# Kernel optimization log

Hardware: AMD Instinct MI355X
Metric: run time of the kernel (lower is better)

## Reference

```python
import jax, jax.numpy as jnp
import numpy as np

B, S, D, H = 2, 2048, 1024, 16
DK = D // H  # 64
EPS = 1e-10
ROPE_BASE = 500000.0


def _rms_norm(x, w):
    # RMSNorm over last dim: w * x / sqrt(mean(x^2) + eps)
    return w * x * jax.lax.rsqrt(jnp.mean(x * x, axis=-1, keepdims=True) + EPS)


def _rope_tables(seq_len, dk):
    inv_freq = 1.0 / (ROPE_BASE ** (jnp.arange(0, dk, 2, dtype=jnp.float32) / dk))
    t = jnp.arange(seq_len, dtype=jnp.float32)
    freqs = jnp.outer(t, inv_freq)            # (S, dk/2)
    emb = jnp.concatenate([freqs, freqs], -1)  # (S, dk)
    return jnp.cos(emb), jnp.sin(emb)


def _rotate_half(x):
    x1, x2 = jnp.split(x, 2, axis=-1)
    return jnp.concatenate([-x2, x1], axis=-1)


def setup_inputs() -> dict:
    key = jax.random.key(0)
    ks = jax.random.split(key, 8)
    scale = 1.0 / np.sqrt(D)
    return {
        "q": jax.random.normal(ks[0], (B, S, D), jnp.float32),
        "k": jax.random.normal(ks[1], (B, S, D), jnp.float32),
        "v": jax.random.normal(ks[2], (B, S, D), jnp.float32),
        "Wq": jax.random.normal(ks[3], (D, D), jnp.float32) * scale,
        "Wk": jax.random.normal(ks[4], (D, D), jnp.float32) * scale,
        "Wv": jax.random.normal(ks[5], (D, D), jnp.float32) * scale,
        "Wo": jax.random.normal(ks[6], (D, D), jnp.float32) * scale,
        "q_norm_w": jnp.ones((DK,), jnp.float32) + 0.02 * jax.random.normal(ks[7], (DK,), jnp.float32),
        "k_norm_w": jnp.ones((DK,), jnp.float32),
    }


def reference(q, k, v, Wq, Wk, Wv, Wo, q_norm_w, k_norm_w):
    Bq, Sq, _ = q.shape
    # Projections (torch Linear: x @ W.T), split into heads -> (B, H, S, DK)
    def proj(x, W):
        return (x @ W.T).reshape(Bq, Sq, H, DK).transpose(0, 2, 1, 3)
    query, key_, value = proj(q, Wq), proj(k, Wk), proj(v, Wv)
    # Per-head QK RMSNorm
    query = _rms_norm(query, q_norm_w)
    key_ = _rms_norm(key_, k_norm_w)
    # RoPE
    cos, sin = _rope_tables(Sq, DK)  # (S, DK) each; broadcast over (B, H)
    query = query * cos + _rotate_half(query) * sin
    key_ = key_ * cos + _rotate_half(key_) * sin
    # Causal attention
    scale = 1.0 / np.sqrt(DK)
    scores = jnp.einsum("bhqd,bhkd->bhqk", query, key_) * scale
    causal = jnp.tril(jnp.ones((Sq, Sq), bool))
    scores = jnp.where(causal, scores, -jnp.inf)
    probs = jax.nn.softmax(scores, axis=-1)
    attn = jnp.einsum("bhqk,bhkd->bhqd", probs, value)
    # Merge heads and output projection
    attn = attn.transpose(0, 2, 1, 3).reshape(Bq, Sq, D)
    return attn @ Wo.T
```

## Files before the change

kernel.cpp:

```cpp
#include <hip/hip_runtime.h>
#include <hip/hip_bf16.h>
#include <math.h>

#define B_  2
#define S_  2048
#define D_  1024
#define H_  16
#define DK_ 64

typedef __attribute__((ext_vector_type(8))) short bf16x8;
typedef __attribute__((ext_vector_type(4))) float f32x4;
typedef __attribute__((ext_vector_type(4))) unsigned int u32x4;

#define MFMA_BF16(a, b, c) __builtin_amdgcn_mfma_f32_16x16x32_bf16((a), (b), (c), 0, 0, 0)

#define QSCALE 0.18033688011112042f
#define ROPE_L2 0.591611512f

__device__ __forceinline__ unsigned short f2bf(float f) {
  unsigned int u = __float_as_uint(f);
  u += 0x7FFFu + ((u >> 16) & 1u);
  return (unsigned short)(u >> 16);
}

__device__ __forceinline__ void gl_lds16(const void* g, void* l) {
  __builtin_amdgcn_global_load_lds(
      (const __attribute__((address_space(1))) void*)g,
      (__attribute__((address_space(3))) void*)l, 16, 0, 0);
}

__device__ __forceinline__ int lsw(int row, int col) {
  return row * 64 + ((((col) >> 3) ^ (row & 7)) << 3) + (col & 7);
}

__device__ __forceinline__ int vperm_inv(int c) {
  return (c & 32) | ((c & 8) << 1) | ((c & 4) << 1) | ((c & 16) >> 2);
}

__global__ __launch_bounds__(256)
void cvt_bf16(const float* __restrict__ q, const float* __restrict__ k,
              const float* __restrict__ v, const float* __restrict__ wq,
              const float* __restrict__ wk, const float* __restrict__ wv,
              const float* __restrict__ wo,
              unsigned short* __restrict__ qb, unsigned short* __restrict__ kb,
              unsigned short* __restrict__ vb, unsigned short* __restrict__ wqb,
              unsigned short* __restrict__ wkb, unsigned short* __restrict__ wvb,
              unsigned short* __restrict__ wob) {
  const float* src; unsigned short* dst; int n;
  switch (blockIdx.y) {
    case 0: src = q;  dst = qb;  n = B_ * S_ * D_; break;
    case 1: src = k;  dst = kb;  n = B_ * S_ * D_; break;
    case 2: src = v;  dst = vb;  n = B_ * S_ * D_; break;
    case 3: src = wq; dst = wqb; n = D_ * D_; break;
    case 4: src = wk; dst = wkb; n = D_ * D_; break;
    case 5: src = wv; dst = wvb; n = D_ * D_; break;
    default: src = wo; dst = wob; n = D_ * D_; break;
  }
  const int i = (blockIdx.x * 256 + threadIdx.x) * 4;
  if (i >= n) return;
  float4 val = *(const float4*)&src[i];
  ushort4 r4;
  r4.x = f2bf(val.x); r4.y = f2bf(val.y); r4.z = f2bf(val.z); r4.w = f2bf(val.w);
  *(ushort4*)&dst[i] = r4;
}

__global__ __launch_bounds__(256)
void gemm_qkv(const unsigned short* __restrict__ qa, const unsigned short* __restrict__ ka,
              const unsigned short* __restrict__ va,
              const unsigned short* __restrict__ wq, const unsigned short* __restrict__ wk,
              const unsigned short* __restrict__ wv,
              unsigned short* __restrict__ Qo, unsigned short* __restrict__ Ko,
              unsigned short* __restrict__ Vto,
              const float* __restrict__ qnw, const float* __restrict__ knw) {
  __shared__ unsigned short As[2][128 * 32];
  __shared__ unsigned short Bs[2][128 * 32];

  const int lin = blockIdx.x + (blockIdx.y << 3) + (blockIdx.z << 8);
  const int v_  = (lin & 7) * 96 + (lin >> 3);
  const int bx  = v_ & 7;
  const int panel = v_ >> 3;
  const int by  = panel & 31;
  const int z   = panel >> 5;

  const unsigned short* A = (z == 0) ? qa : (z == 1) ? ka : va;
  const unsigned short* W = (z == 0) ? wq : (z == 1) ? wk : wv;

  const int t = threadIdx.x, lane = t & 63, wave = t >> 6;
  const int l16 = lane & 15, quad = lane >> 4;
  const int wm = wave >> 1, wn = wave & 1;
  const int m0 = by * 128, j0 = bx * 128;

  f32x4 acc[4][4];
#pragma unroll
  for (int i = 0; i < 4; ++i)
#pragma unroll
    for (int j = 0; j < 4; ++j) acc[i][j] = (f32x4)(0.0f);

  auto stage = [&](int kb, int buf) {
#pragma unroll
    for (int i = 0; i < 2; ++i) {
      const int c  = (wave * 2 + i) * 64 + lane;
      const int r  = c >> 2;
      const int co = (c & 3) * 8;
      gl_lds16(&A[(size_t)(m0 + r) * D_ + kb + co], &As[buf][(wave * 2 + i) * 512]);
      gl_lds16(&W[(size_t)(j0 + r) * D_ + kb + co], &Bs[buf][(wave * 2 + i) * 512]);
    }
  };

  stage(0, 0);
  for (int kb = 0; kb < D_; kb += 32) {
    const int buf = (kb >> 5) & 1;
    __syncthreads();
    if (kb + 32 < D_) stage(kb + 32, buf ^ 1);

    bf16x8 af[4], bfr[4];
#pragma unroll
    for (int mi = 0; mi < 4; ++mi)
      af[mi] = *(const bf16x8*)&As[buf][(wm * 64 + mi * 16 + l16) * 32 + quad * 8];
#pragma unroll
    for (int ni = 0; ni < 4; ++ni)
      bfr[ni] = *(const bf16x8*)&Bs[buf][(wn * 64 + ni * 16 + l16) * 32 + quad * 8];
#pragma unroll
    for (int mi = 0; mi < 4; ++mi)
#pragma unroll
      for (int ni = 0; ni < 4; ++ni)
        acc[mi][ni] = MFMA_BF16(af[mi], bfr[ni], acc[mi][ni]);
  }

  const int h = bx * 2 + wn;
  if (z == 2) {
#pragma unroll
    for (int mi = 0; mi < 4; ++mi) {
      const int rowb = m0 + wm * 64 + mi * 16 + quad * 4;
      const int b = rowb >> 11, s0 = rowb & (S_ - 1);
      const int sp = (s0 & ~63) | vperm_inv(s0 & 63);
#pragma unroll
      for (int ni = 0; ni < 4; ++ni) {
        const int dk = ni * 16 + l16;
        const unsigned int u0 =
            (unsigned int)f2bf(acc[mi][ni][0]) | ((unsigned int)f2bf(acc[mi][ni][1]) << 16);
        const unsigned int u1 =
            (unsigned int)f2bf(acc[mi][ni][2]) | ((unsigned int)f2bf(acc[mi][ni][3]) << 16);
        *(uint2*)&Vto[((size_t)((b * H_ + h) * DK_ + dk)) * S_ + sp] = make_uint2(u0, u1);
      }
    }
  } else {
    unsigned short* out = (z == 0) ? Qo : Ko;
    const float* nw = (z == 0) ? qnw : knw;
    const float sc  = (z == 0) ? QSCALE : 1.0f;
    float wv_[4];
#pragma unroll
    for (int ni = 0; ni < 4; ++ni) wv_[ni] = nw[ni * 16 + l16];
    const float invA = exp2f(-(float)l16 * ROPE_L2);
    const float invB = exp2f(-(float)(16 + l16) * ROPE_L2);
#pragma unroll
    for (int mi = 0; mi < 4; ++mi) {
#pragma unroll
      for (int r = 0; r < 4; ++r) {
        const int rowg = m0 + wm * 64 + mi * 16 + quad * 4 + r;
        const int b = rowg >> 11, s = rowg & (S_ - 1);
        float ss = 0.f;
#pragma unroll
        for (int ni = 0; ni < 4; ++ni) ss += acc[mi][ni][r] * acc[mi][ni][r];
#pragma unroll
        for (int m = 1; m < 16; m <<= 1) ss += __shfl_xor(ss, m);
        const float rms = rsqrtf(ss * (1.0f / DK_) + 1e-10f);
        float xn[4];
#pragma unroll
        for (int ni = 0; ni < 4; ++ni) xn[ni] = wv_[ni] * acc[mi][ni][r] * rms;
        const float fA = (float)s * invA, fB = (float)s * invB;
        const float cA = __cosf(fA) * sc, sA = __sinf(fA) * sc;
        const float cB = __cosf(fB) * sc, sB = __sinf(fB) * sc;
        float o0 = xn[0] * cA - xn[2] * sA;
        float o1 = xn[1] * cB - xn[3] * sB;
        float o2 = xn[2] * cA + xn[0] * sA;
        float o3 = xn[3] * cB + xn[1] * sB;
        const size_t base = ((size_t)(b * H_ + h) * S_ + s) * DK_;
        out[base +  0 + l16] = f2bf(o0);
        out[base + 16 + l16] = f2bf(o1);
        out[base + 32 + l16] = f2bf(o2);
        out[base + 48 + l16] = f2bf(o3);
      }
    }
  }
}

__global__ __launch_bounds__(256)
void flash3(const unsigned short* __restrict__ Q, const unsigned short* __restrict__ K,
            const unsigned short* __restrict__ Vt, unsigned short* __restrict__ Oa) {
  __shared__ unsigned short Ks[2][64 * 64];
  __shared__ unsigned short Vs[3][64 * 64];
  const int bx = blockIdx.x;
  const int idx = bx >> 5;
  const int qt = (idx < 16) ? idx : (47 - idx);
  const int bh = bx & 31;
  const int t = threadIdx.x, lane = t & 63, wave = t >> 6;
  const int l16 = lane & 15, quad = lane >> 4;
  const size_t hb = (size_t)bh * S_ * DK_;
  const unsigned short* Qh  = Q + hb;
  const unsigned short* Kh  = K + hb;
  const unsigned short* Vth = Vt + hb;

  bf16x8 qf[2];
#pragma unroll
  for (int ks = 0; ks < 2; ++ks)
    qf[ks] = *(const bf16x8*)
      &Qh[(size_t)(qt * 64 + wave * 16 + l16) * DK_ + ks * 32 + quad * 8];

  bf16x8 ones;
#pragma unroll
  for (int j = 0; j < 8; ++j) ones[j] = (short)0x3F80;

  f32x4 o[4], lacc;
  lacc = (f32x4)(0.0f);
#pragma unroll
  for (int ni = 0; ni < 4; ++ni) o[ni] = (f32x4)(0.0f);

  auto stage = [&](int kt, int kb_, int vb_) {
#pragma unroll
    for (int i = 0; i < 2; ++i) {
      const int rbase = wave * 16 + i * 8;
      const int r = rbase + (lane >> 3);
      const int c = ((lane & 7) ^ (r & 7)) * 8;
      gl_lds16(&Kh[(size_t)(kt * 64 + r) * DK_ + c], &Ks[kb_][rbase * 64]);
      gl_lds16(&Vth[(size_t)r * S_ + kt * 64 + c], &Vs[vb_][rbase * 64]);
    }
  };

  f32x4 sv[4];

  auto qkt = [&](int kt) {
    const int buf = kt & 1;
#pragma unroll
    for (int kvi = 0; kvi < 4; ++kvi) sv[kvi] = (f32x4)(0.0f);
#pragma unroll
    for (int ks = 0; ks < 2; ++ks) {
      bf16x8 ak[4];
#pragma unroll
      for (int kvi = 0; kvi < 4; ++kvi)
        ak[kvi] = *(const bf16x8*)&Ks[buf][lsw(kvi * 16 + l16, ks * 32 + quad * 8)];
      __builtin_amdgcn_s_setprio(1);
#pragma unroll
      for (int kvi = 0; kvi < 4; ++kvi)
        sv[kvi] = MFMA_BF16(ak[kvi], qf[ks], sv[kvi]);
      __builtin_amdgcn_s_setprio(0);
    }
  };

  auto smx = [&](int kt, unsigned int (&pw)[4][2]) {
    if (kt == qt) {
      const int qg = qt * 64 + wave * 16 + l16;
#pragma unroll
      for (int kvi = 0; kvi < 4; ++kvi) {
        float e[4];
#pragma unroll
        for (int r = 0; r < 4; ++r) {
          float x = sv[kvi][r];
          if ((kt * 64 + kvi * 16 + quad * 4 + r) > qg) x = -INFINITY;
          e[r] = exp2f(x);
        }
        pw[kvi][0] = (__float_as_uint(e[1]) & 0xFFFF0000u) | (__float_as_uint(e[0]) >> 16);
        pw[kvi][1] = (__float_as_uint(e[3]) & 0xFFFF0000u) | (__float_as_uint(e[2]) >> 16);
      }
    } else {
#pragma unroll
      for (int kvi = 0; kvi < 4; ++kvi) {
        float e[4];
#pragma unroll
        for (int r = 0; r < 4; ++r) e[r] = exp2f(sv[kvi][r]);
        pw[kvi][0] = (__float_as_uint(e[1]) & 0xFFFF0000u) | (__float_as_uint(e[0]) >> 16);
        pw[kvi][1] = (__float_as_uint(e[3]) & 0xFFFF0000u) | (__float_as_uint(e[2]) >> 16);
      }
    }
  };

  auto pv = [&](const unsigned int (&pw)[4][2], int vb_) {
    bf16x8 ap[2];
#pragma unroll
    for (int ks = 0; ks < 2; ++ks) {
      u32x4 aw;
      aw.x = pw[2 * ks][0];
      aw.y = pw[2 * ks][1];
      aw.z = pw[2 * ks + 1][0];
      aw.w = pw[2 * ks + 1][1];
      ap[ks] = __builtin_bit_cast(bf16x8, aw);
    }
#pragma unroll
    for (int ks = 0; ks < 2; ++ks) {
      bf16x8 bv[4];
#pragma unroll
      for (int ni = 0; ni < 4; ++ni)
        bv[ni] = *(const bf16x8*)&Vs[vb_][lsw(ni * 16 + l16, ks * 32 + quad * 8)];
      __builtin_amdgcn_s_setprio(1);
#pragma unroll
      for (int ni = 0; ni < 4; ++ni)
        o[ni] = MFMA_BF16(ap[ks], bv[ni], o[ni]);
      lacc = MFMA_BF16(ap[ks], ones, lacc);
      __builtin_amdgcn_s_setprio(0);
    }
  };

  const int nkt = qt + 1;
  unsigned int pwA[4][2], pwB[4][2];

  stage(0, 0, 0);
  __syncthreads();
  if (nkt > 1) stage(1, 1, 1);
  qkt(0);
  smx(0, pwA);

  int kt = 1;
  for (; kt + 1 < nkt; kt += 2) {
    __syncthreads();
    stage(kt + 1, (kt + 1) & 1, (kt + 1) % 3);
    qkt(kt);
    pv(pwA, (kt - 1) % 3);
    smx(kt, pwB);
    __syncthreads();
    if (kt + 2 < nkt) stage(kt + 2, (kt + 2) & 1, (kt + 2) % 3);
    qkt(kt + 1);
    pv(pwB, kt % 3);
    smx(kt + 1, pwA);
  }
  if (kt < nkt) {
    __syncthreads();
    qkt(kt);
    pv(pwA, (kt - 1) % 3);
    smx(kt, pwB);
    pv(pwB, kt % 3);
  } else {
    pv(pwA, (nkt - 1) % 3);
  }

  const int b = bh >> 4, h = bh & 15;
#pragma unroll
  for (int r = 0; r < 4; ++r) {
    const int srow = qt * 64 + wave * 16 + quad * 4 + r;
    const float linv = 1.0f / lacc[r];
#pragma unroll
    for (int ni = 0; ni < 4; ++ni)
      Oa[((size_t)(b * S_ + srow) * H_ + h) * DK_ + ni * 16 + l16] =
          f2bf(o[ni][r] * linv);
  }
}

__global__ __launch_bounds__(256)
void gemm_out(const unsigned short* __restrict__ A, const unsigned short* __restrict__ W,
              float* __restrict__ out) {
  __shared__ unsigned short As[2][128 * 32];
  __shared__ unsigned short Bs[2][128 * 32];
  const int lin = blockIdx.x + (blockIdx.y << 3);
  const int v_  = (lin & 7) * 32 + (lin >> 3);
  const int bx  = v_ & 7;
  const int by  = v_ >> 3;

  const int t = threadIdx.x, lane = t & 63, wave = t >> 6;
  const int l16 = lane & 15, quad = lane >> 4;
  const int wm = wave >> 1, wn = wave & 1;
  const int m0 = by * 128, j0 = bx * 128;

  f32x4 acc[4][4];
#pragma unroll
  for (int i = 0; i < 4; ++i)
#pragma unroll
    for (int j = 0; j < 4; ++j) acc[i][j] = (f32x4)(0.0f);

  auto stage = [&](int kb, int buf) {
#pragma unroll
    for (int i = 0; i < 2; ++i) {
      const int c  = (wave * 2 + i) * 64 + lane;
      const int r  = c >> 2;
      const int co = (c & 3) * 8;
      gl_lds16(&A[(size_t)(m0 + r) * D_ + kb + co], &As[buf][(wave * 2 + i) * 512]);
      gl_lds16(&W[(size_t)(j0 + r) * D_ + kb + co], &Bs[buf][(wave * 2 + i) * 512]);
    }
  };

  stage(0, 0);
  for (int kb = 0; kb < D_; kb += 32) {
    const int buf = (kb >> 5) & 1;
    __syncthreads();
    if (kb + 32 < D_) stage(kb + 32, buf ^ 1);

    bf16x8 af[4], bfr[4];
#pragma unroll
    for (int mi = 0; mi < 4; ++mi)
      af[mi] = *(const bf16x8*)&As[buf][(wm * 64 + mi * 16 + l16) * 32 + quad * 8];
#pragma unroll
    for (int ni = 0; ni < 4; ++ni)
      bfr[ni] = *(const bf16x8*)&Bs[buf][(wn * 64 + ni * 16 + l16) * 32 + quad * 8];
#pragma unroll
    for (int mi = 0; mi < 4; ++mi)
#pragma unroll
      for (int ni = 0; ni < 4; ++ni)
        acc[mi][ni] = MFMA_BF16(af[mi], bfr[ni], acc[mi][ni]);
  }

#pragma unroll
  for (int mi = 0; mi < 4; ++mi) {
    const int rowb = m0 + wm * 64 + mi * 16 + quad * 4;
#pragma unroll
    for (int ni = 0; ni < 4; ++ni) {
      const int col = j0 + wn * 64 + ni * 16 + l16;
#pragma unroll
      for (int r = 0; r < 4; ++r)
        out[(size_t)(rowb + r) * D_ + col] = acc[mi][ni][r];
    }
  }
}

extern "C" void kernel_launch(void* const* d_in, const int* in_sizes, int n_in,
                              void* d_out, int out_size, void* d_ws, size_t ws_size,
                              hipStream_t stream) {
  (void)in_sizes; (void)n_in; (void)out_size; (void)ws_size;
  const float* q  = (const float*)d_in[0];
  const float* k  = (const float*)d_in[1];
  const float* v  = (const float*)d_in[2];
  const float* Wq = (const float*)d_in[3];
  const float* Wk = (const float*)d_in[4];
  const float* Wv = (const float*)d_in[5];
  const float* Wo = (const float*)d_in[6];
  const float* qw = (const float*)d_in[7];
  const float* kw = (const float*)d_in[8];

  char* ws = (char*)d_ws;
  const size_t MB = 1u << 20;
  unsigned short* qb  = (unsigned short*)(ws + 0 * MB);
  unsigned short* kb  = (unsigned short*)(ws + 8 * MB);
  unsigned short* vb  = (unsigned short*)(ws + 16 * MB);
  unsigned short* wqb = (unsigned short*)(ws + 24 * MB);
  unsigned short* wkb = (unsigned short*)(ws + 26 * MB);
  unsigned short* wvb = (unsigned short*)(ws + 28 * MB);
  unsigned short* wob = (unsigned short*)(ws + 30 * MB);
  unsigned short* Qb  = (unsigned short*)(ws + 32 * MB);
  unsigned short* Kb  = (unsigned short*)(ws + 40 * MB);
  unsigned short* Vtb = (unsigned short*)(ws + 48 * MB);
  unsigned short* Ab  = (unsigned short*)(ws + 56 * MB);

  cvt_bf16<<<dim3(4096, 7), 256, 0, stream>>>(q, k, v, Wq, Wk, Wv, Wo,
                                              qb, kb, vb, wqb, wkb, wvb, wob);

  gemm_qkv<<<dim3(D_ / 128, (B_ * S_) / 128, 3), 256, 0, stream>>>(
      qb, kb, vb, wqb, wkb, wvb, Qb, Kb, Vtb, qw, kw);

  flash3<<<1024, 256, 0, stream>>>(Qb, Kb, Vtb, Ab);

  gemm_out<<<dim3(D_ / 128, (B_ * S_) / 128), 256, 0, stream>>>(Ab, wob, (float*)d_out);
}
```

Measured before the change: 203.4 us.

## Fuse fp32-to-bf16 activation conversion into QKV GEMM tile loads

The separate conversion pass over the q/k/v activations is removed. The QKV GEMM now streams fp32 activation tiles directly into a swizzled LDS buffer and converts them to bf16 by truncation when building MFMA fragments. This drops a full read and write of three large activation tensors and the extra kernel work. In exchange the GEMM loads twice as many bytes for A per tile, uses more LDS, and rounds by truncation instead of round-to-nearest.

```diff
diff --git a/kernel.cpp b/kernel.cpp
--- a/kernel.cpp
+++ b/kernel.cpp
@@ -23,6 +23,10 @@
   return (unsigned short)(u >> 16);
 }
 
+__device__ __forceinline__ unsigned int packtr(float e0, float e1) {
+  return (__float_as_uint(e1) & 0xFFFF0000u) | (__float_as_uint(e0) >> 16);
+}
+
 __device__ __forceinline__ void gl_lds16(const void* g, void* l) {
   __builtin_amdgcn_global_load_lds(
       (const __attribute__((address_space(1))) void*)g,
@@ -38,26 +42,18 @@
 }
 
 __global__ __launch_bounds__(256)
-void cvt_bf16(const float* __restrict__ q, const float* __restrict__ k,
-              const float* __restrict__ v, const float* __restrict__ wq,
-              const float* __restrict__ wk, const float* __restrict__ wv,
-              const float* __restrict__ wo,
-              unsigned short* __restrict__ qb, unsigned short* __restrict__ kb,
-              unsigned short* __restrict__ vb, unsigned short* __restrict__ wqb,
-              unsigned short* __restrict__ wkb, unsigned short* __restrict__ wvb,
-              unsigned short* __restrict__ wob) {
-  const float* src; unsigned short* dst; int n;
+void cvt_bf16(const float* __restrict__ wq, const float* __restrict__ wk,
+              const float* __restrict__ wv, const float* __restrict__ wo,
+              unsigned short* __restrict__ wqb, unsigned short* __restrict__ wkb,
+              unsigned short* __restrict__ wvb, unsigned short* __restrict__ wob) {
+  const float* src; unsigned short* dst;
   switch (blockIdx.y) {
-    case 0: src = q;  dst = qb;  n = B_ * S_ * D_; break;
-    case 1: src = k;  dst = kb;  n = B_ * S_ * D_; break;
-    case 2: src = v;  dst = vb;  n = B_ * S_ * D_; break;
-    case 3: src = wq; dst = wqb; n = D_ * D_; break;
-    case 4: src = wk; dst = wkb; n = D_ * D_; break;
-    case 5: src = wv; dst = wvb; n = D_ * D_; break;
-    default: src = wo; dst = wob; n = D_ * D_; break;
+    case 0: src = wq; dst = wqb; break;
+    case 1: src = wk; dst = wkb; break;
+    case 2: src = wv; dst = wvb; break;
+    default: src = wo; dst = wob; break;
   }
   const int i = (blockIdx.x * 256 + threadIdx.x) * 4;
-  if (i >= n) return;
   float4 val = *(const float4*)&src[i];
   ushort4 r4;
   r4.x = f2bf(val.x); r4.y = f2bf(val.y); r4.z = f2bf(val.z); r4.w = f2bf(val.w);
@@ -65,14 +61,14 @@
 }
 
 __global__ __launch_bounds__(256)
-void gemm_qkv(const unsigned short* __restrict__ qa, const unsigned short* __restrict__ ka,
-              const unsigned short* __restrict__ va,
+void gemm_qkv(const float* __restrict__ qa, const float* __restrict__ ka,
+              const float* __restrict__ va,
               const unsigned short* __restrict__ wq, const unsigned short* __restrict__ wk,
               const unsigned short* __restrict__ wv,
               unsigned short* __restrict__ Qo, unsigned short* __restrict__ Ko,
               unsigned short* __restrict__ Vto,
               const float* __restrict__ qnw, const float* __restrict__ knw) {
-  __shared__ unsigned short As[2][128 * 32];
+  __shared__ float          Asf[2][128 * 32];
   __shared__ unsigned short Bs[2][128 * 32];
 
   const int lin = blockIdx.x + (blockIdx.y << 3) + (blockIdx.z << 8);
@@ -82,7 +78,7 @@
   const int by  = panel & 31;
   const int z   = panel >> 5;
 
-  const unsigned short* A = (z == 0) ? qa : (z == 1) ? ka : va;
+  const float* A = (z == 0) ? qa : (z == 1) ? ka : va;
   const unsigned short* W = (z == 0) ? wq : (z == 1) ? wk : wv;
 
   const int t = threadIdx.x, lane = t & 63, wave = t >> 6;
@@ -98,11 +94,17 @@
 
   auto stage = [&](int kb, int buf) {
 #pragma unroll
+    for (int i = 0; i < 4; ++i) {
+      const int c  = i * 256 + t;
+      const int r  = c >> 3;
+      const int cf = (((c & 7) ^ (r & 7)) << 2);
+      gl_lds16(&A[(size_t)(m0 + r) * D_ + kb + cf], &Asf[buf][(c & ~63) << 2]);
+    }
+#pragma unroll
     for (int i = 0; i < 2; ++i) {
       const int c  = (wave * 2 + i) * 64 + lane;
       const int r  = c >> 2;
       const int co = (c & 3) * 8;
-      gl_lds16(&A[(size_t)(m0 + r) * D_ + kb + co], &As[buf][(wave * 2 + i) * 512]);
       gl_lds16(&W[(size_t)(j0 + r) * D_ + kb + co], &Bs[buf][(wave * 2 + i) * 512]);
     }
   };
@@ -115,8 +117,18 @@
 
     bf16x8 af[4], bfr[4];
 #pragma unroll
-    for (int mi = 0; mi < 4; ++mi)
-      af[mi] = *(const bf16x8*)&As[buf][(wm * 64 + mi * 16 + l16) * 32 + quad * 8];
+    for (int mi = 0; mi < 4; ++mi) {
+      const int row = wm * 64 + mi * 16 + l16;
+      const int rb  = row * 32;
+      const f32x4 a0 = *(const f32x4*)&Asf[buf][rb + ((((quad * 2) ^ (row & 7))) << 2)];
+      const f32x4 a1 = *(const f32x4*)&Asf[buf][rb + ((((quad * 2 + 1) ^ (row & 7))) << 2)];
+      u32x4 aw;
+      aw.x = packtr(a0[0], a0[1]);
+      aw.y = packtr(a0[2], a0[3]);
+      aw.z = packtr(a1[0], a1[1]);
+      aw.w = packtr(a1[2], a1[3]);
+      af[mi] = __builtin_bit_cast(bf16x8, aw);
+    }
 #pragma unroll
     for (int ni = 0; ni < 4; ++ni)
       bfr[ni] = *(const bf16x8*)&Bs[buf][(wn * 64 + ni * 16 + l16) * 32 + quad * 8];
@@ -259,8 +271,8 @@
           if ((kt * 64 + kvi * 16 + quad * 4 + r) > qg) x = -INFINITY;
           e[r] = exp2f(x);
         }
-        pw[kvi][0] = (__float_as_uint(e[1]) & 0xFFFF0000u) | (__float_as_uint(e[0]) >> 16);
-        pw[kvi][1] = (__float_as_uint(e[3]) & 0xFFFF0000u) | (__float_as_uint(e[2]) >> 16);
+        pw[kvi][0] = packtr(e[0], e[1]);
+        pw[kvi][1] = packtr(e[2], e[3]);
       }
     } else {
 #pragma unroll
@@ -268,8 +280,8 @@
         float e[4];
 #pragma unroll
         for (int r = 0; r < 4; ++r) e[r] = exp2f(sv[kvi][r]);
-        pw[kvi][0] = (__float_as_uint(e[1]) & 0xFFFF0000u) | (__float_as_uint(e[0]) >> 16);
-        pw[kvi][1] = (__float_as_uint(e[3]) & 0xFFFF0000u) | (__float_as_uint(e[2]) >> 16);
+        pw[kvi][0] = packtr(e[0], e[1]);
+        pw[kvi][1] = packtr(e[2], e[3]);
       }
     }
   };
@@ -425,9 +437,6 @@
 
   char* ws = (char*)d_ws;
   const size_t MB = 1u << 20;
-  unsigned short* qb  = (unsigned short*)(ws + 0 * MB);
-  unsigned short* kb  = (unsigned short*)(ws + 8 * MB);
-  unsigned short* vb  = (unsigned short*)(ws + 16 * MB);
   unsigned short* wqb = (unsigned short*)(ws + 24 * MB);
   unsigned short* wkb = (unsigned short*)(ws + 26 * MB);
   unsigned short* wvb = (unsigned short*)(ws + 28 * MB);
@@ -437,11 +446,11 @@
   unsigned short* Vtb = (unsigned short*)(ws + 48 * MB);
   unsigned short* Ab  = (unsigned short*)(ws + 56 * MB);
 
-  cvt_bf16<<<dim3(4096, 7), 256, 0, stream>>>(q, k, v, Wq, Wk, Wv, Wo,
-                                              qb, kb, vb, wqb, wkb, wvb, wob);
+  cvt_bf16<<<dim3((D_ * D_) / 1024, 4), 256, 0, stream>>>(Wq, Wk, Wv, Wo,
+                                                          wqb, wkb, wvb, wob);
 
   gemm_qkv<<<dim3(D_ / 128, (B_ * S_) / 128, 3), 256, 0, stream>>>(
-      qb, kb, vb, wqb, wkb, wvb, Qb, Kb, Vtb, qw, kw);
+      q, k, v, wqb, wkb, wvb, Qb, Kb, Vtb, qw, kw);
 
   flash3<<<1024, 256, 0, stream>>>(Qb, Kb, Vtb, Ab);
 
```

After: 239.1 us. 1.18x slower.
